# Optimization experiments

Measured on AMD Instinct MI355X. Metric: run time of the kernel, lower is better.

Reference implementation:

```python
import jax, jax.numpy as jnp
import numpy as np

N = 50000
E = 500000
IN_DIM = 384
HID = 256
HEADS = 4
OUT_DIM = 128
NEG_SLOPE = 0.2


def _glorot(key, shape):
    fan_in, fan_out = shape[0], shape[-1]
    lim = jnp.sqrt(6.0 / (fan_in + fan_out))
    return jax.random.uniform(key, shape, jnp.float32, -lim, lim)


def setup_inputs() -> dict:
    key = jax.random.key(0)
    ks = jax.random.split(key, 16)
    x = jax.random.normal(ks[0], (N, IN_DIM), jnp.float32)
    node_attr = jax.random.normal(ks[1], (N, 2), jnp.float32)
    edge_index = jax.random.randint(ks[2], (2, E), 0, N, jnp.int64)
    return {
        "x": x,
        "node_attr": node_attr,
        "edge_index": edge_index,
        # node_encoder: Linear(386 -> 384)
        "enc_W": _glorot(ks[3], (IN_DIM + 2, IN_DIM)),
        "enc_b": jnp.zeros((IN_DIM,), jnp.float32),
        # gat1: 384 -> 4 heads x 256, concat
        "W1": _glorot(ks[4], (IN_DIM, HEADS * HID)),
        "a_src1": _glorot(ks[5], (HEADS, HID)),
        "a_dst1": _glorot(ks[6], (HEADS, HID)),
        "b1": jnp.zeros((HEADS * HID,), jnp.float32),
        # gat2: 1024 -> 1 head x 128, mean (concat=False)
        "W2": _glorot(ks[7], (HEADS * HID, OUT_DIM)),
        "a_src2": _glorot(ks[8], (1, OUT_DIM)),
        "a_dst2": _glorot(ks[9], (1, OUT_DIM)),
        "b2": jnp.zeros((OUT_DIM,), jnp.float32),
    }


def gat_conv(x, src, dst, W, a_src, a_dst, bias, heads, out_ch, concat):
    # x: [N, F]; src/dst: [E'] (self-loops already included)
    n = x.shape[0]
    h = (x @ W).reshape(n, heads, out_ch)          # [N, H, C]
    alpha_s = jnp.einsum('nhc,hc->nh', h, a_src)   # [N, H]
    alpha_d = jnp.einsum('nhc,hc->nh', h, a_dst)
    e = alpha_s[src] + alpha_d[dst]                # [E', H]
    e = jnp.where(e >= 0, e, NEG_SLOPE * e)        # LeakyReLU(0.2)
    # segment softmax over incoming edges of each destination node
    m = jax.ops.segment_max(e, dst, num_segments=n)
    e = jnp.exp(e - m[dst])
    denom = jax.ops.segment_sum(e, dst, num_segments=n)
    alpha = e / (denom[dst] + 1e-16)               # [E', H]
    msg = h[src] * alpha[:, :, None]               # [E', H, C]
    out = jax.ops.segment_sum(msg, dst, num_segments=n)  # [N, H, C]
    out = out.reshape(n, heads * out_ch) if concat else out.mean(axis=1)
    return out + bias


def reference(x, node_attr, edge_index, enc_W, enc_b,
              W1, a_src1, a_dst1, b1, W2, a_src2, a_dst2, b2):
    n = x.shape[0]
    # node encoder on [x ; node_attr]
    h = jnp.concatenate([x, node_attr], axis=-1) @ enc_W + enc_b
    # add self-loops once (PyG GATConv default add_self_loops=True)
    loop = jnp.arange(n, dtype=edge_index.dtype)
    src = jnp.concatenate([edge_index[0], loop])
    dst = jnp.concatenate([edge_index[1], loop])
    h = gat_conv(h, src, dst, W1, a_src1, a_dst1, b1, HEADS, HID, True)
    h = jax.nn.elu(h)
    out = gat_conv(h, src, dst, W2, a_src2, a_dst2, b2, 1, OUT_DIM, False)
    return out
```

## Files before the change

kernel.cpp:

```cpp
#include <hip/hip_runtime.h>
#include <hip/hip_bf16.h>
#include <type_traits>


#define NN 50000
#define NE 500000
#define EP (NE + NN)

typedef __hip_bfloat16 bf16;
typedef short short8 __attribute__((ext_vector_type(8)));
typedef __bf16 bf16x8 __attribute__((ext_vector_type(8)));
typedef float f32x4 __attribute__((ext_vector_type(4)));

__device__ __forceinline__ float b2f(bf16 v) { return __bfloat162float(v); }
__device__ __forceinline__ bf16  f2b(float v) { return __float2bfloat16(v); }
__device__ __forceinline__ unsigned short f2bu(float v) {
  bf16 b = __float2bfloat16(v);
  return *reinterpret_cast<unsigned short*>(&b);
}

__device__ __forceinline__ float ldf(const void* p, size_t i, bool f32) {
  return f32 ? ((const float*)p)[i] : b2f(((const bf16*)p)[i]);
}

__device__ __forceinline__ float bflo(unsigned u) { return __uint_as_float(u << 16); }
__device__ __forceinline__ float bfhi(unsigned u) { return __uint_as_float(u & 0xffff0000u); }

__device__ __forceinline__ float leaky(float v) { return v >= 0.f ? v : 0.2f * v; }

__global__ void k_detect_edge(const unsigned int* __restrict__ w, unsigned int* __restrict__ flag) {
  unsigned int acc = 0;
  for (int i = blockIdx.x * 256 + threadIdx.x; i < NE; i += gridDim.x * 256)
    acc |= w[2 * i + 1];
  if (acc) atomicOr(flag, 1u);
}

__global__ void k_detect_f32(const unsigned int* __restrict__ w, unsigned int* __restrict__ flag) {
  unsigned int acc = 0;
  for (int i = blockIdx.x * 256 + threadIdx.x; i < (1 << 20); i += gridDim.x * 256) {
    unsigned int e = (w[i] >> 7) & 0xFF;
    if (e > 0xA0) acc = 1;
  }
  if (acc) atomicOr(flag, 1u);
}

__global__ void k_convert(const int* __restrict__ ei, const unsigned int* __restrict__ flag,
                          int* __restrict__ esrc, int* __restrict__ edst,
                          int* __restrict__ deg) {
  int e = blockIdx.x * 256 + threadIdx.x;
  if (e >= EP) return;
  int s, d;
  if (e < NE) {
    if (*flag) { s = ei[e]; d = ei[NE + e]; }
    else { const long long* e64 = (const long long*)ei; s = (int)e64[e]; d = (int)e64[NE + e]; }
    s = min(max(s, 0), NN - 1);
    d = min(max(d, 0), NN - 1);
  } else {
    s = d = e - NE;
  }
  esrc[e] = s;
  edst[e] = d;
  atomicAdd(&deg[d], 1);
}

__global__ void k_pack_cat(const void* __restrict__ x, const void* __restrict__ na,
                           bf16* __restrict__ catp, const unsigned int* __restrict__ fflag) {
  const bool f32 = (*fflag != 0);
  const int total = NN * 104;
  for (int g = blockIdx.x * 256 + threadIdx.x; g < total; g += gridDim.x * 256) {
    int n = g / 104, r = g - n * 104;
    int c = r * 4;
    float v0 = 0.f, v1 = 0.f, v2 = 0.f, v3 = 0.f;
    if (c < 384) {
      if (f32) {
        const float4 f = *(const float4*)((const float*)x + (size_t)n * 384 + c);
        v0 = f.x; v1 = f.y; v2 = f.z; v3 = f.w;
      } else {
        const bf16* xb = (const bf16*)x + (size_t)n * 384 + c;
        v0 = b2f(xb[0]); v1 = b2f(xb[1]); v2 = b2f(xb[2]); v3 = b2f(xb[3]);
      }
    } else if (c == 384) {
      v0 = ldf(na, (size_t)n * 2 + 0, f32);
      v1 = ldf(na, (size_t)n * 2 + 1, f32);
    }
    ushort2 o0, o1;
    o0.x = f2bu(v0); o0.y = f2bu(v1);
    o1.x = f2bu(v2); o1.y = f2bu(v3);
    ushort2* dst = (ushort2*)((unsigned short*)catp + (size_t)n * 416 + c);
    dst[0] = o0; dst[1] = o1;
  }
}

__global__ void k_pack_w(const void* __restrict__ W, bf16* __restrict__ Wp,
                         int K, int Kpad, int N, const unsigned int* __restrict__ fflag) {
  const bool f32 = (*fflag != 0);
  int total = Kpad * N;
  for (int i = blockIdx.x * 256 + threadIdx.x; i < total; i += gridDim.x * 256) {
    int kb = i / (N * 32);
    int rem = i - kb * N * 32;
    int n = rem >> 5, kk = rem & 31;
    int k = kb * 32 + kk;
    float v = (k < K) ? ldf(W, (size_t)k * N + n, f32) : 0.f;
    Wp[i] = f2b(v);
  }
}

template<bool ADD_BIAS, bool ALPHA, int NH, typename CT>
__global__ __launch_bounds__(256) void gemm_mfma(
    const bf16* __restrict__ A, int lda,
    const bf16* __restrict__ Bp,
    const void* __restrict__ bias,
    const void* __restrict__ a_srcp, const void* __restrict__ a_dstp,
    float* __restrict__ as_out, float* __restrict__ ad_out,
    CT* __restrict__ C,
    int M, int N, int K,
    const unsigned int* __restrict__ fflag) {
  const bool xf32 = (ADD_BIAS || ALPHA) ? (*fflag != 0) : false;
  __shared__ short As[128 * 40];
  __shared__ short Bs[128 * 40];
  const int t = threadIdx.x;
  const int lane = t & 63, wave = t >> 6;
  const int wm = wave & 1, wn = wave >> 1;
  const int quad = lane >> 4, l15 = lane & 15;
  const int m0 = blockIdx.x * 128, n0 = blockIdx.y * 128;

  f32x4 acc[4][4];
#pragma unroll
  for (int i = 0; i < 4; ++i)
#pragma unroll
    for (int j = 0; j < 4; ++j) acc[i][j] = (f32x4){0.f, 0.f, 0.f, 0.f};

  for (int k0 = 0; k0 < K; k0 += 32) {
#pragma unroll
    for (int i = 0; i < 2; ++i) {
      int c = t + i * 256;
      int row = c >> 2, koff = (c & 3) * 8;
      int gm = min(m0 + row, M - 1);
      const short* src = (const short*)A + (size_t)gm * lda + k0 + koff;
      *(short8*)&As[row * 40 + koff] = *(const short8*)src;
    }
    {
      const short* base = (const short*)Bp + ((size_t)(k0 >> 5) * N + n0) * 32;
#pragma unroll
      for (int i = 0; i < 2; ++i) {
        int c = t + i * 256;
        int nl = c >> 2, koff = (c & 3) * 8;
        *(short8*)&Bs[nl * 40 + koff] = *(const short8*)(base + nl * 32 + koff);
      }
    }
    __syncthreads();
    bf16x8 af[4], bfr[4];
#pragma unroll
    for (int mi = 0; mi < 4; ++mi)
      af[mi] = *reinterpret_cast<const bf16x8*>(&As[(wm * 64 + mi * 16 + l15) * 40 + quad * 8]);
#pragma unroll
    for (int ni = 0; ni < 4; ++ni)
      bfr[ni] = *reinterpret_cast<const bf16x8*>(&Bs[(wn * 64 + ni * 16 + l15) * 40 + quad * 8]);
#pragma unroll
    for (int mi = 0; mi < 4; ++mi)
#pragma unroll
      for (int ni = 0; ni < 4; ++ni)
        acc[mi][ni] = __builtin_amdgcn_mfma_f32_16x16x32_bf16(af[mi], bfr[ni], acc[mi][ni], 0, 0, 0);
    __syncthreads();
  }

#pragma unroll
  for (int mi = 0; mi < 4; ++mi) {
#pragma unroll
    for (int ni = 0; ni < 4; ++ni) {
      const int gn = n0 + wn * 64 + ni * 16 + l15;
      float bv = ADD_BIAS ? ldf(bias, gn, xf32) : 0.f;
#pragma unroll
      for (int r = 0; r < 4; ++r) {
        const int gm = m0 + wm * 64 + mi * 16 + quad * 4 + r;
        if (gm < M) {
          float v = acc[mi][ni][r] + bv;
          if constexpr (std::is_same<CT, float>::value)
            C[(size_t)gm * N + gn] = v;
          else
            C[(size_t)gm * N + gn] = f2b(v);
        }
      }
    }
  }

  if (ALPHA) {
    float avs[4], avd[4];
#pragma unroll
    for (int ni = 0; ni < 4; ++ni) {
      const int gn = n0 + wn * 64 + ni * 16 + l15;
      avs[ni] = ldf(a_srcp, gn, xf32);
      avd[ni] = ldf(a_dstp, gn, xf32);
    }
    const int head = (n0 + wn * 64) >> 8;
#pragma unroll
    for (int mi = 0; mi < 4; ++mi) {
#pragma unroll
      for (int r = 0; r < 4; ++r) {
        float ps = 0.f, pd = 0.f;
#pragma unroll
        for (int ni = 0; ni < 4; ++ni) {
          const float v = acc[mi][ni][r];
          ps = fmaf(v, avs[ni], ps);
          pd = fmaf(v, avd[ni], pd);
        }
#pragma unroll
        for (int off = 8; off > 0; off >>= 1) {
          ps += __shfl_down(ps, off, 16);
          pd += __shfl_down(pd, off, 16);
        }
        if (l15 == 0) {
          const int gm = m0 + wm * 64 + mi * 16 + quad * 4 + r;
          if (gm < M) {
            atomicAdd(&as_out[gm * NH + head], ps);
            atomicAdd(&ad_out[gm * NH + head], pd);
          }
        }
      }
    }
  }
}

#define SCAN_B 512
#define SCAN_NB ((NN + SCAN_B - 1) / SCAN_B)

__global__ __launch_bounds__(SCAN_B) void k_scan1(const int* __restrict__ deg,
                                                  int* __restrict__ row_ptr,
                                                  int* __restrict__ partial) {
  int b = blockIdx.x, t = threadIdx.x;
  int i = b * SCAN_B + t;
  int v = (i < NN) ? deg[i] : 0;
  int lane = t & 63, w = t >> 6;
  int x = v;
#pragma unroll
  for (int off = 1; off < 64; off <<= 1) {
    int y = __shfl_up(x, off, 64);
    if (lane >= off) x += y;
  }
  __shared__ int ws[8];
  if (lane == 63) ws[w] = x;
  __syncthreads();
  if (t == 0) {
    int run = 0;
#pragma unroll
    for (int j = 0; j < 8; ++j) { int tmp = ws[j]; ws[j] = run; run += tmp; }
    partial[b] = run;
  }
  __syncthreads();
  int excl = x - v + ws[w];
  if (i < NN) row_ptr[i] = excl;
}

__global__ void k_scan2(int* __restrict__ partial, int* __restrict__ row_ptr) {
  if (blockIdx.x == 0 && threadIdx.x == 0) {
    int run = 0;
    for (int j = 0; j < SCAN_NB; ++j) { int tmp = partial[j]; partial[j] = run; run += tmp; }
    row_ptr[NN] = run;
  }
}

__global__ __launch_bounds__(SCAN_B) void k_scan3(const int* __restrict__ partial,
                                                  int* __restrict__ row_ptr,
                                                  int* __restrict__ cursor) {
  int b = blockIdx.x, t = threadIdx.x;
  int i = b * SCAN_B + t;
  if (i < NN) {
    int v = row_ptr[i] + partial[b];
    row_ptr[i] = v;
    cursor[i] = v;
  }
}

__global__ void k_scatter(const int* __restrict__ esrc, const int* __restrict__ edst,
                          int* __restrict__ cursor, int* __restrict__ csr) {
  int e = blockIdx.x * 256 + threadIdx.x;
  if (e >= EP) return;
  int pos = atomicAdd(&cursor[edst[e]], 1);
  pos = min(max(pos, 0), EP - 1);
  csr[pos] = esrc[e];
}

__global__ __launch_bounds__(256) void k_agg1(
    const int* __restrict__ csr, const int* __restrict__ row_ptr,
    const float* __restrict__ as1, const float* __restrict__ ad1,
    const bf16* __restrict__ h1, const void* __restrict__ b1,
    bf16* __restrict__ act1, const unsigned int* __restrict__ fflag) {
  const bool f32 = (*fflag != 0);
  const int n = blockIdx.x, t = threadIdx.x;
  const int w = t >> 6, l = t & 63;
  const int start = row_ptr[n], end = row_ptr[n + 1];
  const float adn = ad1[n * 4 + w];
  const unsigned* hb = (const unsigned*)h1;
  const int coff = w * 128 + l * 2;

  float a0 = 0.f, a1 = 0.f, a2 = 0.f, a3 = 0.f, densum = 0.f;

  int idx = start;
  for (; idx + 4 <= end; idx += 4) {
    int s0 = csr[idx], s1 = csr[idx + 1], s2 = csr[idx + 2], s3 = csr[idx + 3];
    uint2 w0 = *(const uint2*)(hb + (size_t)s0 * 512 + coff);
    uint2 w1 = *(const uint2*)(hb + (size_t)s1 * 512 + coff);
    uint2 w2 = *(const uint2*)(hb + (size_t)s2 * 512 + coff);
    uint2 w3 = *(const uint2*)(hb + (size_t)s3 * 512 + coff);
    float p0 = __expf(leaky(as1[s0 * 4 + w] + adn));
    float p1 = __expf(leaky(as1[s1 * 4 + w] + adn));
    float p2 = __expf(leaky(as1[s2 * 4 + w] + adn));
    float p3 = __expf(leaky(as1[s3 * 4 + w] + adn));
    densum += (p0 + p1) + (p2 + p3);
    a0 = fmaf(bflo(w0.x), p0, a0); a1 = fmaf(bfhi(w0.x), p0, a1);
    a2 = fmaf(bflo(w0.y), p0, a2); a3 = fmaf(bfhi(w0.y), p0, a3);
    a0 = fmaf(bflo(w1.x), p1, a0); a1 = fmaf(bfhi(w1.x), p1, a1);
    a2 = fmaf(bflo(w1.y), p1, a2); a3 = fmaf(bfhi(w1.y), p1, a3);
    a0 = fmaf(bflo(w2.x), p2, a0); a1 = fmaf(bfhi(w2.x), p2, a1);
    a2 = fmaf(bflo(w2.y), p2, a2); a3 = fmaf(bfhi(w2.y), p2, a3);
    a0 = fmaf(bflo(w3.x), p3, a0); a1 = fmaf(bfhi(w3.x), p3, a1);
    a2 = fmaf(bflo(w3.y), p3, a2); a3 = fmaf(bfhi(w3.y), p3, a3);
  }
  for (; idx < end; ++idx) {
    int s0 = csr[idx];
    uint2 w0 = *(const uint2*)(hb + (size_t)s0 * 512 + coff);
    float p0 = __expf(leaky(as1[s0 * 4 + w] + adn));
    densum += p0;
    a0 = fmaf(bflo(w0.x), p0, a0); a1 = fmaf(bfhi(w0.x), p0, a1);
    a2 = fmaf(bflo(w0.y), p0, a2); a3 = fmaf(bfhi(w0.y), p0, a3);
  }

  const float inv = 1.f / (densum + 1e-16f);
  const int col = w * 256 + l * 4;
  float v0 = a0 * inv + ldf(b1, col + 0, f32);
  float v1 = a1 * inv + ldf(b1, col + 1, f32);
  float v2 = a2 * inv + ldf(b1, col + 2, f32);
  float v3 = a3 * inv + ldf(b1, col + 3, f32);
  v0 = v0 > 0.f ? v0 : expm1f(v0);
  v1 = v1 > 0.f ? v1 : expm1f(v1);
  v2 = v2 > 0.f ? v2 : expm1f(v2);
  v3 = v3 > 0.f ? v3 : expm1f(v3);
  unsigned lo = (unsigned)f2bu(v0) | ((unsigned)f2bu(v1) << 16);
  unsigned hi = (unsigned)f2bu(v2) | ((unsigned)f2bu(v3) << 16);
  unsigned long long ow = (unsigned long long)lo | ((unsigned long long)hi << 32);
  __builtin_nontemporal_store(
      ow, (unsigned long long*)((unsigned short*)act1 + (size_t)n * 1024 + col));
}

__global__ __launch_bounds__(256) void k_agg2(
    const int* __restrict__ csr, const int* __restrict__ row_ptr,
    const float* __restrict__ as2, const float* __restrict__ ad2,
    const bf16* __restrict__ h2, const void* __restrict__ b2v,
    float* __restrict__ out, const unsigned int* __restrict__ fflag) {
  const bool f32 = (*fflag != 0);
  const int t = threadIdx.x;
  const int wv = t >> 6, l = t & 63;
  const int n = blockIdx.x * 4 + wv;
  const int start = row_ptr[n], end = row_ptr[n + 1];
  const float adn = ad2[n];
  const unsigned* hb = (const unsigned*)h2;
  float a0 = 0.f, a1 = 0.f, densum = 0.f;

  int idx = start;
  for (; idx + 2 <= end; idx += 2) {
    const int s0 = __builtin_amdgcn_readfirstlane(csr[idx]);
    const int s1 = __builtin_amdgcn_readfirstlane(csr[idx + 1]);
    const unsigned w0 = hb[(size_t)s0 * 64 + l];
    const unsigned w1 = hb[(size_t)s1 * 64 + l];
    const float p0 = __expf(leaky(as2[s0] + adn));
    const float p1 = __expf(leaky(as2[s1] + adn));
    densum += p0 + p1;
    a0 = fmaf(bflo(w0), p0, a0); a1 = fmaf(bfhi(w0), p0, a1);
    a0 = fmaf(bflo(w1), p1, a0); a1 = fmaf(bfhi(w1), p1, a1);
  }
  if (idx < end) {
    const int s0 = __builtin_amdgcn_readfirstlane(csr[idx]);
    const unsigned w0 = hb[(size_t)s0 * 64 + l];
    const float p0 = __expf(leaky(as2[s0] + adn));
    densum += p0;
    a0 = fmaf(bflo(w0), p0, a0); a1 = fmaf(bfhi(w0), p0, a1);
  }

  const float inv = 1.f / (densum + 1e-16f);
  float2 o;
  o.x = a0 * inv + ldf(b2v, l * 2 + 0, f32);
  o.y = a1 * inv + ldf(b2v, l * 2 + 1, f32);
  unsigned long long u;
  __builtin_memcpy(&u, &o, 8);
  __builtin_nontemporal_store(u, (unsigned long long*)(out + (size_t)n * 128 + l * 2));
}

extern "C" void kernel_launch(void* const* d_in, const int* in_sizes, int n_in,
                              void* d_out, int out_size, void* d_ws, size_t ws_size,
                              hipStream_t stream) {
  const void* x       = d_in[0];
  const void* na      = d_in[1];
  const int*  ei      = (const int*)d_in[2];
  const void* enc_W   = d_in[3];
  const void* enc_b   = d_in[4];
  const void* W1      = d_in[5];
  const void* a_src1  = d_in[6];
  const void* a_dst1  = d_in[7];
  const void* b1      = d_in[8];
  const void* W2      = d_in[9];
  const void* a_src2  = d_in[10];
  const void* a_dst2  = d_in[11];
  const void* b2      = d_in[12];
  float* out = (float*)d_out;

  size_t off = 0;
  char* ws = (char*)d_ws;
  auto alloc = [&](size_t bytes) -> void* {
    void* p = ws + off;
    off += (bytes + 255) & ~(size_t)255;
    return p;
  };
  bf16*  h1      = (bf16*)alloc((size_t)NN * 1024 * 2);
  bf16*  act1    = (bf16*)alloc((size_t)NN * 1024 * 2);
  bf16*  catp    = act1;
  bf16*  h0      = (bf16*)alloc((size_t)NN * 384 * 2);
  bf16*  h2      = (bf16*)alloc((size_t)NN * 128 * 2);
  bf16*  encWp   = (bf16*)alloc((size_t)416 * 384 * 2);
  bf16*  W1p     = (bf16*)alloc((size_t)384 * 1024 * 2);
  bf16*  W2p     = (bf16*)alloc((size_t)1024 * 128 * 2);
  int*   esrc    = (int*)alloc((size_t)EP * 4);
  int*   edst    = (int*)alloc((size_t)EP * 4);
  unsigned int* eflag = (unsigned int*)alloc(4);
  unsigned int* fflag = (unsigned int*)alloc(4);
  int*   csr     = (int*)alloc((size_t)EP * 4);
  float* as1     = (float*)alloc((size_t)NN * 4 * 4);
  float* ad1     = (float*)alloc((size_t)NN * 4 * 4);
  float* as2     = (float*)alloc((size_t)NN * 4);
  float* ad2     = (float*)alloc((size_t)NN * 4);
  int*   deg     = (int*)alloc((size_t)NN * 4);
  int*   row_ptr = (int*)alloc((size_t)(NN + 1) * 4);
  int*   cursor  = (int*)alloc((size_t)NN * 4);
  int*   partial = (int*)alloc((size_t)SCAN_NB * 4);
  (void)ws_size; (void)in_sizes; (void)n_in; (void)out_size;

  (void)hipMemsetAsync(eflag, 0, 4,               stream);
  (void)hipMemsetAsync(fflag, 0, 4,               stream);
  (void)hipMemsetAsync(deg,   0, (size_t)NN * 4,  stream);
  (void)hipMemsetAsync(as1,   0, (size_t)NN * 16, stream);
  (void)hipMemsetAsync(ad1,   0, (size_t)NN * 16, stream);
  (void)hipMemsetAsync(as2,   0, (size_t)NN * 4,  stream);
  (void)hipMemsetAsync(ad2,   0, (size_t)NN * 4,  stream);

  const int EB = (EP + 255) / 256;
  const int MB = (NN + 127) / 128;

  k_detect_edge<<<512, 256, 0, stream>>>((const unsigned int*)ei, eflag);
  k_detect_f32<<<512, 256, 0, stream>>>((const unsigned int*)x, fflag);

  k_convert<<<EB, 256, 0, stream>>>(ei, eflag, esrc, edst, deg);
  k_scan1<<<SCAN_NB, SCAN_B, 0, stream>>>(deg, row_ptr, partial);
  k_scan2<<<1, 64, 0, stream>>>(partial, row_ptr);
  k_scan3<<<SCAN_NB, SCAN_B, 0, stream>>>(partial, row_ptr, cursor);
  k_scatter<<<EB, 256, 0, stream>>>(esrc, edst, cursor, csr);

  k_pack_cat<<<8192, 256, 0, stream>>>(x, na, catp, fflag);
  k_pack_w<<<1024, 256, 0, stream>>>(enc_W, encWp, 386, 416, 384, fflag);
  k_pack_w<<<1024, 256, 0, stream>>>(W1, W1p, 384, 384, 1024, fflag);
  k_pack_w<<<1024, 256, 0, stream>>>(W2, W2p, 1024, 1024, 128, fflag);

  gemm_mfma<true, false, 1, bf16><<<dim3(MB, 3), 256, 0, stream>>>(
      catp, 416, encWp, enc_b, nullptr, nullptr, nullptr, nullptr,
      h0, NN, 384, 416, fflag);
  gemm_mfma<false, true, 4, bf16><<<dim3(MB, 8), 256, 0, stream>>>(
      h0, 384, W1p, nullptr, a_src1, a_dst1, as1, ad1,
      h1, NN, 1024, 384, fflag);

  k_agg1<<<NN, 256, 0, stream>>>(csr, row_ptr, as1, ad1, h1, b1, act1, fflag);

  gemm_mfma<false, true, 1, bf16><<<dim3(MB, 1), 256, 0, stream>>>(
      act1, 1024, W2p, nullptr, a_src2, a_dst2, as2, ad2,
      h2, NN, 128, 1024, fflag);

  k_agg2<<<NN / 4, 256, 0, stream>>>(csr, row_ptr, as2, ad2, h2, b2, out, fflag);
}
```

Measured before the change: 695.2 us.

## Fold encoder weights into first GAT projection to eliminate the encoder GEMM

Precomposes enc_W @ W1 into a single 386x1024 weight with a small GEMM each call. It also folds enc_b into a composed bias, enc_b @ W1. The big layer-1 GEMM then runs directly on the packed [x; node_attr] input with K=416, removing the 50000x384 intermediate h0 along with its write and read traffic and one large GEMM launch. The composed bias is added both to h1 and to the attention-logit dot products. Costs are a few small setup kernels and different bf16 rounding, since composed weights are quantized once and the h0 rounding step is gone.

After: 747.5 us. 1.08x slower.

```diff
diff --git a/kernel.cpp b/kernel.cpp
--- a/kernel.cpp
+++ b/kernel.cpp
@@ -91,6 +91,24 @@
   }
 }
 
+__global__ void k_cvt(const void* __restrict__ src, bf16* __restrict__ dst, int total,
+                      const unsigned int* __restrict__ fflag) {
+  const bool f32 = (*fflag != 0);
+  for (int i = blockIdx.x * 256 + threadIdx.x; i < total; i += gridDim.x * 256)
+    dst[i] = f2b(ldf(src, i, f32));
+}
+
+__global__ void k_bias_compose(const void* __restrict__ enc_b, const void* __restrict__ W1,
+                               float* __restrict__ bc, const unsigned int* __restrict__ fflag) {
+  const bool f32 = (*fflag != 0);
+  int n = blockIdx.x * 256 + threadIdx.x;
+  if (n >= 1024) return;
+  float s = 0.f;
+  for (int j = 0; j < 384; ++j)
+    s = fmaf(ldf(enc_b, j, f32), ldf(W1, (size_t)j * 1024 + n, f32), s);
+  bc[n] = s;
+}
+
 __global__ void k_pack_w(const void* __restrict__ W, bf16* __restrict__ Wp,
                          int K, int Kpad, int N, const unsigned int* __restrict__ fflag) {
   const bool f32 = (*fflag != 0);
@@ -105,7 +123,7 @@
   }
 }
 
-template<bool ADD_BIAS, bool ALPHA, int NH, typename CT>
+template<bool ADD_BIAS, bool ALPHA, bool BIAS_F32, int NH, typename CT>
 __global__ __launch_bounds__(256) void gemm_mfma(
     const bf16* __restrict__ A, int lda,
     const bf16* __restrict__ Bp,
@@ -169,7 +187,9 @@
 #pragma unroll
     for (int ni = 0; ni < 4; ++ni) {
       const int gn = n0 + wn * 64 + ni * 16 + l15;
-      float bv = ADD_BIAS ? ldf(bias, gn, xf32) : 0.f;
+      float bv = 0.f;
+      if constexpr (ADD_BIAS)
+        bv = BIAS_F32 ? ((const float*)bias)[gn] : ldf(bias, gn, xf32);
 #pragma unroll
       for (int r = 0; r < 4; ++r) {
         const int gm = m0 + wm * 64 + mi * 16 + quad * 4 + r;
@@ -185,12 +205,16 @@
   }
 
   if (ALPHA) {
-    float avs[4], avd[4];
+    float avs[4], avd[4], bvs[4];
 #pragma unroll
     for (int ni = 0; ni < 4; ++ni) {
       const int gn = n0 + wn * 64 + ni * 16 + l15;
       avs[ni] = ldf(a_srcp, gn, xf32);
       avd[ni] = ldf(a_dstp, gn, xf32);
+      if constexpr (ADD_BIAS)
+        bvs[ni] = BIAS_F32 ? ((const float*)bias)[gn] : ldf(bias, gn, xf32);
+      else
+        bvs[ni] = 0.f;
     }
     const int head = (n0 + wn * 64) >> 8;
 #pragma unroll
@@ -200,7 +224,7 @@
         float ps = 0.f, pd = 0.f;
 #pragma unroll
         for (int ni = 0; ni < 4; ++ni) {
-          const float v = acc[mi][ni][r];
+          const float v = acc[mi][ni][r] + bvs[ni];
           ps = fmaf(v, avs[ni], ps);
           pd = fmaf(v, avd[ni], pd);
         }
@@ -413,15 +437,18 @@
   bf16*  h1      = (bf16*)alloc((size_t)NN * 1024 * 2);
   bf16*  act1    = (bf16*)alloc((size_t)NN * 1024 * 2);
   bf16*  catp    = act1;
-  bf16*  h0      = (bf16*)alloc((size_t)NN * 384 * 2);
   bf16*  h2      = (bf16*)alloc((size_t)NN * 128 * 2);
-  bf16*  encWp   = (bf16*)alloc((size_t)416 * 384 * 2);
+  bf16*  encA    = (bf16*)alloc((size_t)386 * 384 * 2);
+  float* Wc      = (float*)alloc((size_t)386 * 1024 * 4);
+  bf16*  Wcp     = (bf16*)alloc((size_t)416 * 1024 * 2);
+  float* bc      = (float*)alloc((size_t)1024 * 4);
   bf16*  W1p     = (bf16*)alloc((size_t)384 * 1024 * 2);
   bf16*  W2p     = (bf16*)alloc((size_t)1024 * 128 * 2);
   int*   esrc    = (int*)alloc((size_t)EP * 4);
   int*   edst    = (int*)alloc((size_t)EP * 4);
   unsigned int* eflag = (unsigned int*)alloc(4);
   unsigned int* fflag = (unsigned int*)alloc(4);
+  unsigned int* oneflag = (unsigned int*)alloc(4);
   int*   csr     = (int*)alloc((size_t)EP * 4);
   float* as1     = (float*)alloc((size_t)NN * 4 * 4);
   float* ad1     = (float*)alloc((size_t)NN * 4 * 4);
@@ -435,6 +462,7 @@
 
   (void)hipMemsetAsync(eflag, 0, 4,               stream);
   (void)hipMemsetAsync(fflag, 0, 4,               stream);
+  (void)hipMemsetAsync(oneflag, 1, 4,             stream);
   (void)hipMemsetAsync(deg,   0, (size_t)NN * 4,  stream);
   (void)hipMemsetAsync(as1,   0, (size_t)NN * 16, stream);
   (void)hipMemsetAsync(ad1,   0, (size_t)NN * 16, stream);
@@ -453,21 +481,24 @@
   k_scan3<<<SCAN_NB, SCAN_B, 0, stream>>>(partial, row_ptr, cursor);
   k_scatter<<<EB, 256, 0, stream>>>(esrc, edst, cursor, csr);
 
+  k_pack_w<<<1024, 256, 0, stream>>>(W1, W1p, 384, 384, 1024, fflag);
+  k_pack_w<<<256, 256, 0, stream>>>(W2, W2p, 1024, 1024, 128, fflag);
+  k_cvt<<<579, 256, 0, stream>>>(enc_W, encA, 386 * 384, fflag);
+  k_bias_compose<<<4, 256, 0, stream>>>(enc_b, W1, bc, fflag);
+  gemm_mfma<false, false, false, 1, float><<<dim3(4, 8), 256, 0, stream>>>(
+      encA, 384, W1p, nullptr, nullptr, nullptr, nullptr, nullptr,
+      Wc, 386, 1024, 384, fflag);
+  k_pack_w<<<1024, 256, 0, stream>>>(Wc, Wcp, 386, 416, 1024, oneflag);
+
   k_pack_cat<<<8192, 256, 0, stream>>>(x, na, catp, fflag);
-  k_pack_w<<<1024, 256, 0, stream>>>(enc_W, encWp, 386, 416, 384, fflag);
-  k_pack_w<<<1024, 256, 0, stream>>>(W1, W1p, 384, 384, 1024, fflag);
-  k_pack_w<<<1024, 256, 0, stream>>>(W2, W2p, 1024, 1024, 128, fflag);
-
-  gemm_mfma<true, false, 1, bf16><<<dim3(MB, 3), 256, 0, stream>>>(
-      catp, 416, encWp, enc_b, nullptr, nullptr, nullptr, nullptr,
-      h0, NN, 384, 416, fflag);
-  gemm_mfma<false, true, 4, bf16><<<dim3(MB, 8), 256, 0, stream>>>(
-      h0, 384, W1p, nullptr, a_src1, a_dst1, as1, ad1,
-      h1, NN, 1024, 384, fflag);
+
+  gemm_mfma<true, true, true, 4, bf16><<<dim3(MB, 8), 256, 0, stream>>>(
+      catp, 416, Wcp, bc, a_src1, a_dst1, as1, ad1,
+      h1, NN, 1024, 416, fflag);
 
   k_agg1<<<NN, 256, 0, stream>>>(csr, row_ptr, as1, ad1, h1, b1, act1, fflag);
 
-  gemm_mfma<false, true, 1, bf16><<<dim3(MB, 1), 256, 0, stream>>>(
+  gemm_mfma<false, true, false, 1, bf16><<<dim3(MB, 1), 256, 0, stream>>>(
       act1, 1024, W2p, nullptr, a_src2, a_dst2, as2, ad2,
       h2, NN, 128, 1024, fflag);
 
```
